# Optimization experiments

Hardware: AMD Instinct MI355X
Metric: run time of the kernel (lower is better)

The kernel has to match this reference:

```python
import jax, jax.numpy as jnp
import numpy as np

NQ, NL, PD, B = 4, 2, 64, 524288
RANGES = [1, 2]  # StronglyEntanglingLayers default: (l % (nq-1)) + 1


def setup_inputs() -> dict:
    key = jax.random.key(0)
    ks = jax.random.split(key, 4)
    x = jax.random.normal(ks[0], (B, NQ), jnp.float32)
    # PennyLane TorchLayer default init: uniform [0, 2pi)
    weights = jax.random.uniform(ks[1], (NL, NQ, 3), jnp.float32, 0.0, 2.0 * np.pi)
    W = jax.random.normal(ks[2], (PD, NQ), jnp.float32) / np.sqrt(NQ)
    b = jnp.zeros((PD,), jnp.float32)
    gamma = jnp.ones((PD,), jnp.float32)
    beta = jnp.zeros((PD,), jnp.float32)
    return {"x": x, "weights": weights, "W": W, "b": b, "gamma": gamma, "beta": beta}


def _apply_1q_batched(state, gate, w):
    # state: [B, 2,2,2,2], gate: [B,2,2], act on wire w (axis w+1)
    s = jnp.moveaxis(state, w + 1, -1)
    s = jnp.einsum('bij,b...j->b...i', gate, s)
    return jnp.moveaxis(s, -1, w + 1)


def _apply_1q_shared(state, gate, w):
    s = jnp.moveaxis(state, w + 1, -1)
    s = jnp.einsum('ij,b...j->b...i', gate, s)
    return jnp.moveaxis(s, -1, w + 1)


def _cnot(state, c, t):
    s = jnp.moveaxis(state, (c + 1, t + 1), (-2, -1))
    s = jnp.stack([s[..., 0, :], s[..., 1, ::-1]], axis=-2)  # flip target where control=1
    return jnp.moveaxis(s, (-2, -1), (c + 1, t + 1))


def _rot(phi, theta, omega):
    # Rot = RZ(omega) RY(theta) RZ(phi)
    ct, st = jnp.cos(theta / 2), jnp.sin(theta / 2)
    ep = jnp.exp(-0.5j * (phi + omega))
    em = jnp.exp(-0.5j * (phi - omega))
    return jnp.array([[ep * ct, -jnp.conj(em) * st],
                      [em * st, jnp.conj(ep) * ct]])


def _circuit(x, weights):
    n = x.shape[0]
    state = jnp.zeros((n,) + (2,) * NQ, jnp.complex64)
    state = state.at[(slice(None),) + (0,) * NQ].set(1.0)
    # AngleEmbedding (RX rotations)
    half = x * 0.5
    c, s = jnp.cos(half), jnp.sin(half)
    for w in range(NQ):
        cw, sw = c[:, w], -1j * s[:, w]
        g = jnp.stack([jnp.stack([cw + 0j, sw], -1),
                       jnp.stack([sw, cw + 0j], -1)], -2)  # [B,2,2]
        state = _apply_1q_batched(state, g, w)
    # StronglyEntanglingLayers
    for l in range(NL):
        for w in range(NQ):
            state = _apply_1q_shared(state, _rot(weights[l, w, 0], weights[l, w, 1], weights[l, w, 2]), w)
        r = RANGES[l]
        for w in range(NQ):
            state = _cnot(state, w, (w + r) % NQ)
    probs = state.real ** 2 + state.imag ** 2  # [B,2,2,2,2]
    zs = []
    for w in range(NQ):
        other = tuple(a for a in range(1, NQ + 1) if a != w + 1)
        m = probs.sum(other)  # [B,2]
        zs.append(m[:, 0] - m[:, 1])  # <Z_w>
    return jnp.stack(zs, -1)  # [B,4]


def reference(x, weights, W, b, gamma, beta):
    xt = jnp.tanh(x) * jnp.pi
    q = _circuit(xt, weights)
    q = jax.nn.softmax(q, axis=-1)
    h = q @ W.T + b  # [B, 64]
    mu = h.mean(-1, keepdims=True)
    var = ((h - mu) ** 2).mean(-1, keepdims=True)
    return (h - mu) / jnp.sqrt(var + 1e-5) * gamma + beta
```

## Files before the change

kernel.cpp:

```cpp
#include <hip/hip_runtime.h>

#define BLK 256
#define PD 64
#define PI_F 3.14159265358979323846f

__device__ __forceinline__ float fast_tanh(float v) {
    float e = __expf(2.0f * v);
    return 1.0f - 2.0f / (e + 1.0f);
}

extern "C" __global__ void __launch_bounds__(BLK)
qbranch_kernel(const float* __restrict__ x,
               const float* __restrict__ wts,
               const float* __restrict__ W,
               const float* __restrict__ bias,
               const float* __restrict__ gamma,
               const float* __restrict__ beta,
               float* __restrict__ out)
{
    __shared__ float sg[64];
    __shared__ float sS[20];
    __shared__ float sq[BLK][9];

    const int t = threadIdx.x;
    const int b = blockIdx.x * BLK + t;

    const float4 xv = reinterpret_cast<const float4*>(x)[b];
    const int p4 = t & 15;
    const float4 w0 = reinterpret_cast<const float4*>(W)[p4 * 4 + 0];
    const float4 w1 = reinterpret_cast<const float4*>(W)[p4 * 4 + 1];
    const float4 w2 = reinterpret_cast<const float4*>(W)[p4 * 4 + 2];
    const float4 w3 = reinterpret_cast<const float4*>(W)[p4 * 4 + 3];
    const float4 bg = reinterpret_cast<const float4*>(bias)[p4];
    const float4 gm = reinterpret_cast<const float4*>(gamma)[p4];
    const float4 bt = reinterpret_cast<const float4*>(beta)[p4];

    if (t < 64) {
        const float4 wr = reinterpret_cast<const float4*>(W)[t];
        const float bp = bias[t];
        float v[20] = { wr.x*wr.x, wr.x*wr.y, wr.x*wr.z, wr.x*wr.w,
                        wr.y*wr.y, wr.y*wr.z, wr.y*wr.w,
                        wr.z*wr.z, wr.z*wr.w,
                        wr.w*wr.w,
                        wr.x*bp, wr.y*bp, wr.z*bp, wr.w*bp,
                        wr.x, wr.y, wr.z, wr.w,
                        bp, bp*bp };
        #pragma unroll
        for (int o = 32; o > 0; o >>= 1) {
            #pragma unroll
            for (int k = 0; k < 20; ++k) v[k] += __shfl_xor(v[k], o, 64);
        }
        if (t == 0) {
            #pragma unroll
            for (int k = 0; k < 20; ++k) sS[k] = v[k] * (1.0f / 64.0f);
        }
    } else if (t < 72) {
        const int g = t - 64, l = g >> 2, w = g & 3;
        const float phi = wts[(l * 4 + w) * 3 + 0];
        const float th  = wts[(l * 4 + w) * 3 + 1];
        const float om  = wts[(l * 4 + w) * 3 + 2];
        float st, ct;  __sincosf(0.5f * th, &st, &ct);
        float sa, ca;  __sincosf(0.5f * (phi + om), &sa, &ca);
        float sb, cb;  __sincosf(0.5f * (phi - om), &sb, &cb);
        float* gg = &sg[g * 8];
        gg[0] =  ct * ca;  gg[1] = -ct * sa;
        gg[2] = -st * cb;  gg[3] = -st * sb;
        gg[4] =  st * cb;  gg[5] = -st * sb;
        gg[6] =  ct * ca;  gg[7] =  ct * sa;
    }

    float cc[4], ss[4];
    {
        const float xs[4] = {xv.x, xv.y, xv.z, xv.w};
        #pragma unroll
        for (int w = 0; w < 4; ++w) {
            const float xt = fast_tanh(xs[w]) * PI_F;
            __sincosf(0.5f * xt, &ss[w], &cc[w]);
        }
    }
    float ar[16], ai[16];
    #pragma unroll
    for (int i = 0; i < 16; ++i) {
        float m = 1.0f;
        #pragma unroll
        for (int w = 0; w < 4; ++w)
            m *= ((i >> (3 - w)) & 1) ? ss[w] : cc[w];
        const int k = __popc((unsigned)i) & 3;
        ar[i] = (k == 0) ? m : (k == 2 ? -m : 0.0f);
        ai[i] = (k == 1) ? -m : (k == 3 ? m : 0.0f);
    }

    __syncthreads();

    #pragma unroll
    for (int l = 0; l < 2; ++l) {
        #pragma unroll
        for (int w = 0; w < 4; ++w) {
            const float* gg = &sg[(l * 4 + w) * 8];
            const float u00r = gg[0], u00i = gg[1], u01r = gg[2], u01i = gg[3];
            const float u10r = gg[4], u10i = gg[5], u11r = gg[6], u11i = gg[7];
            const int m = 1 << (3 - w);
            #pragma unroll
            for (int i = 0; i < 16; ++i) {
                if (i & m) continue;
                const int j = i | m;
                const float a0r = ar[i], a0i = ai[i], a1r = ar[j], a1i = ai[j];
                ar[i] = u00r*a0r - u00i*a0i + u01r*a1r - u01i*a1i;
                ai[i] = u00r*a0i + u00i*a0r + u01r*a1i + u01i*a1r;
                ar[j] = u10r*a0r - u10i*a0i + u11r*a1r - u11i*a1i;
                ai[j] = u10r*a0i + u10i*a0r + u11r*a1i + u11i*a1r;
            }
        }
        const int r = (l == 0) ? 1 : 2;
        #pragma unroll
        for (int w = 0; w < 4; ++w) {
            const int cm = 1 << (3 - w);
            const int tq = (w + r) & 3;
            const int tm = 1 << (3 - tq);
            #pragma unroll
            for (int i = 0; i < 16; ++i) {
                if ((i & cm) && !(i & tm)) {
                    const int j = i | tm;
                    float tp;
                    tp = ar[i]; ar[i] = ar[j]; ar[j] = tp;
                    tp = ai[i]; ai[i] = ai[j]; ai[j] = tp;
                }
            }
        }
    }

    float z0 = 0.f, z1 = 0.f, z2 = 0.f, z3 = 0.f;
    #pragma unroll
    for (int i = 0; i < 16; ++i) {
        const float p = ar[i]*ar[i] + ai[i]*ai[i];
        z0 += (i & 8) ? -p : p;
        z1 += (i & 4) ? -p : p;
        z2 += (i & 2) ? -p : p;
        z3 += (i & 1) ? -p : p;
    }
    const float mx = fmaxf(fmaxf(z0, z1), fmaxf(z2, z3));
    const float e0 = __expf(z0 - mx), e1 = __expf(z1 - mx);
    const float e2 = __expf(z2 - mx), e3 = __expf(z3 - mx);
    const float inv = 1.0f / (e0 + e1 + e2 + e3);
    const float q0 = e0 * inv, q1 = e1 * inv, q2 = e2 * inv, q3 = e3 * inv;

    const float mu = fmaf(q0, sS[14], fmaf(q1, sS[15], fmaf(q2, sS[16], fmaf(q3, sS[17], sS[18]))));
    const float t0 = sS[0]*q0 + sS[1]*q1 + sS[2]*q2 + sS[3]*q3 + 2.0f*sS[10];
    const float t1 = sS[1]*q0 + sS[4]*q1 + sS[5]*q2 + sS[6]*q3 + 2.0f*sS[11];
    const float t2 = sS[2]*q0 + sS[5]*q1 + sS[7]*q2 + sS[8]*q3 + 2.0f*sS[12];
    const float t3 = sS[3]*q0 + sS[6]*q1 + sS[8]*q2 + sS[9]*q3 + 2.0f*sS[13];
    const float Eh2 = t0*q0 + t1*q1 + t2*q2 + t3*q3 + sS[19];
    const float var = Eh2 - mu * mu;
    const float rstd = rsqrtf(var + 1e-5f);

    sq[t][0] = q0; sq[t][1] = q1; sq[t][2] = q2; sq[t][3] = q3;
    sq[t][4] = mu; sq[t][5] = rstd;
    __syncthreads();

    const int sub = t >> 4;
    const size_t base = (size_t)blockIdx.x * (BLK * PD);
    #pragma unroll 4
    for (int it = 0; it < 16; ++it) {
        const int row = it * 16 + sub;
        const float r0 = sq[row][0], r1 = sq[row][1], r2 = sq[row][2], r3 = sq[row][3];
        const float mur = sq[row][4], rsr = sq[row][5];
        const float h0 = fmaf(r0, w0.x, fmaf(r1, w0.y, fmaf(r2, w0.z, fmaf(r3, w0.w, bg.x))));
        const float h1 = fmaf(r0, w1.x, fmaf(r1, w1.y, fmaf(r2, w1.z, fmaf(r3, w1.w, bg.y))));
        const float h2 = fmaf(r0, w2.x, fmaf(r1, w2.y, fmaf(r2, w2.z, fmaf(r3, w2.w, bg.z))));
        const float h3 = fmaf(r0, w3.x, fmaf(r1, w3.y, fmaf(r2, w3.z, fmaf(r3, w3.w, bg.w))));
        float4 pk;
        pk.x = fmaf((h0 - mur), rsr * gm.x, bt.x);
        pk.y = fmaf((h1 - mur), rsr * gm.y, bt.y);
        pk.z = fmaf((h2 - mur), rsr * gm.z, bt.z);
        pk.w = fmaf((h3 - mur), rsr * gm.w, bt.w);
        *reinterpret_cast<float4*>(&out[base + (size_t)row * PD + p4 * 4]) = pk;
    }
}

extern "C" void kernel_launch(void* const* d_in, const int* in_sizes, int n_in,
                              void* d_out, int out_size, void* d_ws, size_t ws_size,
                              hipStream_t stream) {
    const float* x     = (const float*)d_in[0];
    const float* wts   = (const float*)d_in[1];
    const float* W     = (const float*)d_in[2];
    const float* bias  = (const float*)d_in[3];
    const float* gamma = (const float*)d_in[4];
    const float* beta  = (const float*)d_in[5];
    float* out = (float*)d_out;
    const int B = in_sizes[0] / 4;
    hipLaunchKernelGGL(qbranch_kernel, dim3(B / BLK), dim3(BLK), 0, stream,
                       x, wts, W, bias, gamma, beta, out);
}
```

Baseline: 185.9 us.

## Hoist gate and LayerNorm stats into prep kernel; fold first layer into product state

Moves the per-block computation of the Rot gate matrices and the W/bias second-moment statistics into a separate one-block prep kernel that writes them to workspace. The main kernel reads them from global memory. It also folds the RX embedding and first Rot layer into per-qubit 2-vectors, because the state is still a product state before any CNOT, and builds the 16-amplitude state via tensor products. This removes four full gate applications and the redundant per-block setup work and syncs, at the cost of an extra kernel launch and uniform global loads. The shared staging is also switched to float4/float2 layout.

```diff
diff --git a/kernel.cpp b/kernel.cpp
--- a/kernel.cpp
+++ b/kernel.cpp
@@ -9,23 +9,166 @@
     return 1.0f - 2.0f / (e + 1.0f);
 }
 
+template<int M>
+__device__ __forceinline__ void gate_apply(float* ar, float* ai,
+        float u00r, float u00i, float u01r, float u01i,
+        float u10r, float u10i, float u11r, float u11i) {
+    #pragma unroll
+    for (int i = 0; i < 16; ++i) {
+        if (i & M) continue;
+        const int j = i | M;
+        const float a0r = ar[i], a0i = ai[i], a1r = ar[j], a1i = ai[j];
+        ar[i] = u00r*a0r - u00i*a0i + u01r*a1r - u01i*a1i;
+        ai[i] = u00r*a0i + u00i*a0r + u01r*a1i + u01i*a1r;
+        ar[j] = u10r*a0r - u10i*a0i + u11r*a1r - u11i*a1i;
+        ai[j] = u10r*a0i + u10i*a0r + u11r*a1i + u11i*a1r;
+    }
+}
+
+template<int CM, int TM>
+__device__ __forceinline__ void cnotg(float* ar, float* ai) {
+    #pragma unroll
+    for (int i = 0; i < 16; ++i) {
+        if ((i & CM) && !(i & TM)) {
+            const int j = i | TM;
+            float tp;
+            tp = ar[i]; ar[i] = ar[j]; ar[j] = tp;
+            tp = ai[i]; ai[i] = ai[j]; ai[j] = tp;
+        }
+    }
+}
+
+extern "C" __global__ void __launch_bounds__(64)
+qbranch_prep(const float* __restrict__ wts, const float* __restrict__ W,
+             const float* __restrict__ bias, float* __restrict__ ws)
+{
+    const int t = threadIdx.x;
+    const float4 wr = reinterpret_cast<const float4*>(W)[t];
+    const float bp = bias[t];
+    float v[20] = { wr.x*wr.x, wr.x*wr.y, wr.x*wr.z, wr.x*wr.w,
+                    wr.y*wr.y, wr.y*wr.z, wr.y*wr.w,
+                    wr.z*wr.z, wr.z*wr.w,
+                    wr.w*wr.w,
+                    wr.x*bp, wr.y*bp, wr.z*bp, wr.w*bp,
+                    wr.x, wr.y, wr.z, wr.w,
+                    bp, bp*bp };
+    #pragma unroll
+    for (int o = 32; o > 0; o >>= 1) {
+        #pragma unroll
+        for (int k = 0; k < 20; ++k) v[k] += __shfl_xor(v[k], o, 64);
+    }
+    if (t == 0) {
+        #pragma unroll
+        for (int k = 0; k < 20; ++k) ws[64 + k] = v[k] * (1.0f / 64.0f);
+    }
+    if (t < 8) {
+        const float phi = wts[t * 3 + 0];
+        const float th  = wts[t * 3 + 1];
+        const float om  = wts[t * 3 + 2];
+        float st, ct;  __sincosf(0.5f * th, &st, &ct);
+        float sa, ca;  __sincosf(0.5f * (phi + om), &sa, &ca);
+        float sb, cb;  __sincosf(0.5f * (phi - om), &sb, &cb);
+        float* gg = ws + t * 8;
+        gg[0] =  ct * ca;  gg[1] = -ct * sa;
+        gg[2] = -st * cb;  gg[3] = -st * sb;
+        gg[4] =  st * cb;  gg[5] = -st * sb;
+        gg[6] =  ct * ca;  gg[7] =  ct * sa;
+    }
+}
+
 extern "C" __global__ void __launch_bounds__(BLK)
-qbranch_kernel(const float* __restrict__ x,
-               const float* __restrict__ wts,
-               const float* __restrict__ W,
-               const float* __restrict__ bias,
-               const float* __restrict__ gamma,
-               const float* __restrict__ beta,
-               float* __restrict__ out)
+qbranch_main(const float* __restrict__ x,
+             const float* __restrict__ W,
+             const float* __restrict__ bias,
+             const float* __restrict__ gamma,
+             const float* __restrict__ beta,
+             const float* __restrict__ cw,
+             float* __restrict__ out)
 {
-    __shared__ float sg[64];
-    __shared__ float sS[20];
-    __shared__ float sq[BLK][9];
+    __shared__ float4 sq4[BLK];
+    __shared__ float2 sms[BLK];
 
     const int t = threadIdx.x;
     const int b = blockIdx.x * BLK + t;
-
     const float4 xv = reinterpret_cast<const float4*>(x)[b];
+
+    float v0r[4], v0i[4], v1r[4], v1i[4];
+    const float xs[4] = {xv.x, xv.y, xv.z, xv.w};
+    #pragma unroll
+    for (int w = 0; w < 4; ++w) {
+        float s, c;
+        __sincosf(0.5f * PI_F * fast_tanh(xs[w]), &s, &c);
+        const float g0 = cw[w*8+0], g1 = cw[w*8+1], g2 = cw[w*8+2], g3 = cw[w*8+3];
+        const float g4 = cw[w*8+4], g5 = cw[w*8+5], g6 = cw[w*8+6], g7 = cw[w*8+7];
+        v0r[w] = fmaf(c, g0,  s * g3);
+        v0i[w] = fmaf(c, g1, -s * g2);
+        v1r[w] = fmaf(c, g4,  s * g7);
+        v1i[w] = fmaf(c, g5, -s * g6);
+    }
+
+    float Ar[4], Ai[4], Br[4], Bi[4];
+    #pragma unroll
+    for (int j = 0; j < 4; ++j) {
+        const int b0 = j >> 1, b1 = j & 1;
+        const float p0r = b0 ? v1r[0] : v0r[0], p0i = b0 ? v1i[0] : v0i[0];
+        const float p1r = b1 ? v1r[1] : v0r[1], p1i = b1 ? v1i[1] : v0i[1];
+        Ar[j] = p0r*p1r - p0i*p1i;
+        Ai[j] = p0r*p1i + p0i*p1r;
+        const float p2r = b0 ? v1r[2] : v0r[2], p2i = b0 ? v1i[2] : v0i[2];
+        const float p3r = b1 ? v1r[3] : v0r[3], p3i = b1 ? v1i[3] : v0i[3];
+        Br[j] = p2r*p3r - p2i*p3i;
+        Bi[j] = p2r*p3i + p2i*p3r;
+    }
+    float ar[16], ai[16];
+    #pragma unroll
+    for (int i = 0; i < 16; ++i) {
+        const int hi = i >> 2, lo = i & 3;
+        ar[i] = Ar[hi]*Br[lo] - Ai[hi]*Bi[lo];
+        ai[i] = Ar[hi]*Bi[lo] + Ai[hi]*Br[lo];
+    }
+
+    cnotg<8, 4>(ar, ai);
+    cnotg<4, 2>(ar, ai);
+    cnotg<2, 1>(ar, ai);
+    cnotg<1, 8>(ar, ai);
+
+    gate_apply<8>(ar, ai, cw[32], cw[33], cw[34], cw[35], cw[36], cw[37], cw[38], cw[39]);
+    gate_apply<4>(ar, ai, cw[40], cw[41], cw[42], cw[43], cw[44], cw[45], cw[46], cw[47]);
+    gate_apply<2>(ar, ai, cw[48], cw[49], cw[50], cw[51], cw[52], cw[53], cw[54], cw[55]);
+    gate_apply<1>(ar, ai, cw[56], cw[57], cw[58], cw[59], cw[60], cw[61], cw[62], cw[63]);
+
+    cnotg<8, 2>(ar, ai);
+    cnotg<4, 1>(ar, ai);
+    cnotg<2, 8>(ar, ai);
+    cnotg<1, 4>(ar, ai);
+
+    float z0 = 0.f, z1 = 0.f, z2 = 0.f, z3 = 0.f;
+    #pragma unroll
+    for (int i = 0; i < 16; ++i) {
+        const float p = ar[i]*ar[i] + ai[i]*ai[i];
+        z0 += (i & 8) ? -p : p;
+        z1 += (i & 4) ? -p : p;
+        z2 += (i & 2) ? -p : p;
+        z3 += (i & 1) ? -p : p;
+    }
+    const float mx = fmaxf(fmaxf(z0, z1), fmaxf(z2, z3));
+    const float e0 = __expf(z0 - mx), e1 = __expf(z1 - mx);
+    const float e2 = __expf(z2 - mx), e3 = __expf(z3 - mx);
+    const float inv = 1.0f / (e0 + e1 + e2 + e3);
+    const float q0 = e0 * inv, q1 = e1 * inv, q2 = e2 * inv, q3 = e3 * inv;
+
+    const float* sS = cw + 64;
+    const float mu = fmaf(q0, sS[14], fmaf(q1, sS[15], fmaf(q2, sS[16], fmaf(q3, sS[17], sS[18]))));
+    const float t0 = sS[0]*q0 + sS[1]*q1 + sS[2]*q2 + sS[3]*q3 + 2.0f*sS[10];
+    const float t1 = sS[1]*q0 + sS[4]*q1 + sS[5]*q2 + sS[6]*q3 + 2.0f*sS[11];
+    const float t2 = sS[2]*q0 + sS[5]*q1 + sS[7]*q2 + sS[8]*q3 + 2.0f*sS[12];
+    const float t3 = sS[3]*q0 + sS[6]*q1 + sS[8]*q2 + sS[9]*q3 + 2.0f*sS[13];
+    const float Eh2 = t0*q0 + t1*q1 + t2*q2 + t3*q3 + sS[19];
+    const float rstd = rsqrtf(Eh2 - mu * mu + 1e-5f);
+
+    sq4[t] = make_float4(q0, q1, q2, q3);
+    sms[t] = make_float2(mu, rstd);
+
     const int p4 = t & 15;
     const float4 w0 = reinterpret_cast<const float4*>(W)[p4 * 4 + 0];
     const float4 w1 = reinterpret_cast<const float4*>(W)[p4 * 4 + 1];
@@ -35,126 +178,6 @@
     const float4 gm = reinterpret_cast<const float4*>(gamma)[p4];
     const float4 bt = reinterpret_cast<const float4*>(beta)[p4];
 
-    if (t < 64) {
-        const float4 wr = reinterpret_cast<const float4*>(W)[t];
-        const float bp = bias[t];
-        float v[20] = { wr.x*wr.x, wr.x*wr.y, wr.x*wr.z, wr.x*wr.w,
-                        wr.y*wr.y, wr.y*wr.z, wr.y*wr.w,
-                        wr.z*wr.z, wr.z*wr.w,
-                        wr.w*wr.w,
-                        wr.x*bp, wr.y*bp, wr.z*bp, wr.w*bp,
-                        wr.x, wr.y, wr.z, wr.w,
-                        bp, bp*bp };
-        #pragma unroll
-        for (int o = 32; o > 0; o >>= 1) {
-            #pragma unroll
-            for (int k = 0; k < 20; ++k) v[k] += __shfl_xor(v[k], o, 64);
-        }
-        if (t == 0) {
-            #pragma unroll
-            for (int k = 0; k < 20; ++k) sS[k] = v[k] * (1.0f / 64.0f);
-        }
-    } else if (t < 72) {
-        const int g = t - 64, l = g >> 2, w = g & 3;
-        const float phi = wts[(l * 4 + w) * 3 + 0];
-        const float th  = wts[(l * 4 + w) * 3 + 1];
-        const float om  = wts[(l * 4 + w) * 3 + 2];
-        float st, ct;  __sincosf(0.5f * th, &st, &ct);
-        float sa, ca;  __sincosf(0.5f * (phi + om), &sa, &ca);
-        float sb, cb;  __sincosf(0.5f * (phi - om), &sb, &cb);
-        float* gg = &sg[g * 8];
-        gg[0] =  ct * ca;  gg[1] = -ct * sa;
-        gg[2] = -st * cb;  gg[3] = -st * sb;
-        gg[4] =  st * cb;  gg[5] = -st * sb;
-        gg[6] =  ct * ca;  gg[7] =  ct * sa;
-    }
-
-    float cc[4], ss[4];
-    {
-        const float xs[4] = {xv.x, xv.y, xv.z, xv.w};
-        #pragma unroll
-        for (int w = 0; w < 4; ++w) {
-            const float xt = fast_tanh(xs[w]) * PI_F;
-            __sincosf(0.5f * xt, &ss[w], &cc[w]);
-        }
-    }
-    float ar[16], ai[16];
-    #pragma unroll
-    for (int i = 0; i < 16; ++i) {
-        float m = 1.0f;
-        #pragma unroll
-        for (int w = 0; w < 4; ++w)
-            m *= ((i >> (3 - w)) & 1) ? ss[w] : cc[w];
-        const int k = __popc((unsigned)i) & 3;
-        ar[i] = (k == 0) ? m : (k == 2 ? -m : 0.0f);
-        ai[i] = (k == 1) ? -m : (k == 3 ? m : 0.0f);
-    }
-
-    __syncthreads();
-
-    #pragma unroll
-    for (int l = 0; l < 2; ++l) {
-        #pragma unroll
-        for (int w = 0; w < 4; ++w) {
-            const float* gg = &sg[(l * 4 + w) * 8];
-            const float u00r = gg[0], u00i = gg[1], u01r = gg[2], u01i = gg[3];
-            const float u10r = gg[4], u10i = gg[5], u11r = gg[6], u11i = gg[7];
-            const int m = 1 << (3 - w);
-            #pragma unroll
-            for (int i = 0; i < 16; ++i) {
-                if (i & m) continue;
-                const int j = i | m;
-                const float a0r = ar[i], a0i = ai[i], a1r = ar[j], a1i = ai[j];
-                ar[i] = u00r*a0r - u00i*a0i + u01r*a1r - u01i*a1i;
-                ai[i] = u00r*a0i + u00i*a0r + u01r*a1i + u01i*a1r;
-                ar[j] = u10r*a0r - u10i*a0i + u11r*a1r - u11i*a1i;
-                ai[j] = u10r*a0i + u10i*a0r + u11r*a1i + u11i*a1r;
-            }
-        }
-        const int r = (l == 0) ? 1 : 2;
-        #pragma unroll
-        for (int w = 0; w < 4; ++w) {
-            const int cm = 1 << (3 - w);
-            const int tq = (w + r) & 3;
-            const int tm = 1 << (3 - tq);
-            #pragma unroll
-            for (int i = 0; i < 16; ++i) {
-                if ((i & cm) && !(i & tm)) {
-                    const int j = i | tm;
-                    float tp;
-                    tp = ar[i]; ar[i] = ar[j]; ar[j] = tp;
-                    tp = ai[i]; ai[i] = ai[j]; ai[j] = tp;
-                }
-            }
-        }
-    }
-
-    float z0 = 0.f, z1 = 0.f, z2 = 0.f, z3 = 0.f;
-    #pragma unroll
-    for (int i = 0; i < 16; ++i) {
-        const float p = ar[i]*ar[i] + ai[i]*ai[i];
-        z0 += (i & 8) ? -p : p;
-        z1 += (i & 4) ? -p : p;
-        z2 += (i & 2) ? -p : p;
-        z3 += (i & 1) ? -p : p;
-    }
-    const float mx = fmaxf(fmaxf(z0, z1), fmaxf(z2, z3));
-    const float e0 = __expf(z0 - mx), e1 = __expf(z1 - mx);
-    const float e2 = __expf(z2 - mx), e3 = __expf(z3 - mx);
-    const float inv = 1.0f / (e0 + e1 + e2 + e3);
-    const float q0 = e0 * inv, q1 = e1 * inv, q2 = e2 * inv, q3 = e3 * inv;
-
-    const float mu = fmaf(q0, sS[14], fmaf(q1, sS[15], fmaf(q2, sS[16], fmaf(q3, sS[17], sS[18]))));
-    const float t0 = sS[0]*q0 + sS[1]*q1 + sS[2]*q2 + sS[3]*q3 + 2.0f*sS[10];
-    const float t1 = sS[1]*q0 + sS[4]*q1 + sS[5]*q2 + sS[6]*q3 + 2.0f*sS[11];
-    const float t2 = sS[2]*q0 + sS[5]*q1 + sS[7]*q2 + sS[8]*q3 + 2.0f*sS[12];
-    const float t3 = sS[3]*q0 + sS[6]*q1 + sS[8]*q2 + sS[9]*q3 + 2.0f*sS[13];
-    const float Eh2 = t0*q0 + t1*q1 + t2*q2 + t3*q3 + sS[19];
-    const float var = Eh2 - mu * mu;
-    const float rstd = rsqrtf(var + 1e-5f);
-
-    sq[t][0] = q0; sq[t][1] = q1; sq[t][2] = q2; sq[t][3] = q3;
-    sq[t][4] = mu; sq[t][5] = rstd;
     __syncthreads();
 
     const int sub = t >> 4;
@@ -162,17 +185,17 @@
     #pragma unroll 4
     for (int it = 0; it < 16; ++it) {
         const int row = it * 16 + sub;
-        const float r0 = sq[row][0], r1 = sq[row][1], r2 = sq[row][2], r3 = sq[row][3];
-        const float mur = sq[row][4], rsr = sq[row][5];
-        const float h0 = fmaf(r0, w0.x, fmaf(r1, w0.y, fmaf(r2, w0.z, fmaf(r3, w0.w, bg.x))));
-        const float h1 = fmaf(r0, w1.x, fmaf(r1, w1.y, fmaf(r2, w1.z, fmaf(r3, w1.w, bg.y))));
-        const float h2 = fmaf(r0, w2.x, fmaf(r1, w2.y, fmaf(r2, w2.z, fmaf(r3, w2.w, bg.z))));
-        const float h3 = fmaf(r0, w3.x, fmaf(r1, w3.y, fmaf(r2, w3.z, fmaf(r3, w3.w, bg.w))));
+        const float4 qv = sq4[row];
+        const float2 ms = sms[row];
+        const float h0 = fmaf(qv.x, w0.x, fmaf(qv.y, w0.y, fmaf(qv.z, w0.z, fmaf(qv.w, w0.w, bg.x))));
+        const float h1 = fmaf(qv.x, w1.x, fmaf(qv.y, w1.y, fmaf(qv.z, w1.z, fmaf(qv.w, w1.w, bg.y))));
+        const float h2 = fmaf(qv.x, w2.x, fmaf(qv.y, w2.y, fmaf(qv.z, w2.z, fmaf(qv.w, w2.w, bg.z))));
+        const float h3 = fmaf(qv.x, w3.x, fmaf(qv.y, w3.y, fmaf(qv.z, w3.z, fmaf(qv.w, w3.w, bg.w))));
         float4 pk;
-        pk.x = fmaf((h0 - mur), rsr * gm.x, bt.x);
-        pk.y = fmaf((h1 - mur), rsr * gm.y, bt.y);
-        pk.z = fmaf((h2 - mur), rsr * gm.z, bt.z);
-        pk.w = fmaf((h3 - mur), rsr * gm.w, bt.w);
+        pk.x = fmaf((h0 - ms.x), ms.y * gm.x, bt.x);
+        pk.y = fmaf((h1 - ms.x), ms.y * gm.y, bt.y);
+        pk.z = fmaf((h2 - ms.x), ms.y * gm.z, bt.z);
+        pk.w = fmaf((h3 - ms.x), ms.y * gm.w, bt.w);
         *reinterpret_cast<float4*>(&out[base + (size_t)row * PD + p4 * 4]) = pk;
     }
 }
@@ -186,8 +209,10 @@
     const float* bias  = (const float*)d_in[3];
     const float* gamma = (const float*)d_in[4];
     const float* beta  = (const float*)d_in[5];
+    float* ws  = (float*)d_ws;
     float* out = (float*)d_out;
     const int B = in_sizes[0] / 4;
-    hipLaunchKernelGGL(qbranch_kernel, dim3(B / BLK), dim3(BLK), 0, stream,
-                       x, wts, W, bias, gamma, beta, out);
-}
+    hipLaunchKernelGGL(qbranch_prep, dim3(1), dim3(64), 0, stream, wts, W, bias, ws);
+    hipLaunchKernelGGL(qbranch_main, dim3(B / BLK), dim3(BLK), 0, stream,
+                       x, W, bias, gamma, beta, ws, out);
+}
```

Result: faster. 175.4 us (-5.7%).
